# Performance work log

Measured on AMD Instinct MI355X. Metric: run time of the kernel, lower is better.

The kernel has to match this reference:

```python
import jax, jax.numpy as jnp
import numpy as np
from jax import lax

BS, T, D, HID, N = 256, 128, 256, 256, 15


def _gru_layer(x, Wih, Whh, bih, bhh):
    # x: (bs, T, in). PyTorch GRU cell math, gates ordered [r, z, n].
    h0 = jnp.zeros((x.shape[0], Whh.shape[1]), x.dtype)

    def step(h, x_t):
        gi = x_t @ Wih.T + bih
        gh = h @ Whh.T + bhh
        ir, iz, inn = jnp.split(gi, 3, axis=-1)
        hr, hz, hn = jnp.split(gh, 3, axis=-1)
        r = jax.nn.sigmoid(ir + hr)
        z = jax.nn.sigmoid(iz + hz)
        n = jnp.tanh(inn + r * hn)
        h = (1.0 - z) * n + z * h
        return h, h

    _, hs = lax.scan(step, h0, jnp.swapaxes(x, 0, 1))  # (T, bs, H)
    return jnp.swapaxes(hs, 0, 1)


def setup_inputs() -> dict:
    key = jax.random.key(0)
    ks = jax.random.split(key, 14)
    s = 0.08
    inp = {
        'P': jax.random.normal(ks[0], (BS, T, D), jnp.float32),
        'Wih0': jax.random.normal(ks[1], (3 * HID, D), jnp.float32) * s,
        'Whh0': jax.random.normal(ks[2], (3 * HID, HID), jnp.float32) * s,
        'bih0': jax.random.normal(ks[3], (3 * HID,), jnp.float32) * s,
        'bhh0': jax.random.normal(ks[4], (3 * HID,), jnp.float32) * s,
        'Wih1': jax.random.normal(ks[5], (3 * HID, HID), jnp.float32) * s,
        'Whh1': jax.random.normal(ks[6], (3 * HID, HID), jnp.float32) * s,
        'bih1': jax.random.normal(ks[7], (3 * HID,), jnp.float32) * s,
        'bhh1': jax.random.normal(ks[8], (3 * HID,), jnp.float32) * s,
        'W': jax.random.normal(ks[9], (D, HID), jnp.float32) * s,
        'Wp1': jax.random.normal(ks[10], (HID, HID), jnp.float32) * s,
        'Wp2': jax.random.normal(ks[11], (1, HID), jnp.float32) * s,
        'Wr1': jax.random.normal(ks[12], (HID, HID), jnp.float32) * s,
        'Wr2': jax.random.normal(ks[13], (D, HID), jnp.float32) * s,
    }
    # Precomputed derangement negatives: cyclic shift by k in [1, bs-1]
    # guarantees neg_idx[t, n, b] != b (matches the original assert).
    rng = np.random.default_rng(0)
    shifts = rng.integers(1, BS, size=(T - 1, N))
    neg_idx = (np.arange(BS)[None, None, :] + shifts[:, :, None]) % BS
    inp['neg_idx'] = jnp.asarray(neg_idx, jnp.int32)  # (T-1, N, bs)
    return inp


def reference(P, Wih0, Whh0, bih0, bhh0, Wih1, Whh1, bih1, bhh1,
              W, Wp1, Wp2, Wr1, Wr2, neg_idx):
    # 2-layer GRU temporal encoder
    H1 = _gru_layer(P, Wih0, Whh0, bih0, bhh0)
    H = _gru_layer(H1, Wih1, Whh1, bih1, bhh1)  # (bs, T, HID)

    # Contrastive loss over timesteps t = 1..T-1 (vectorized)
    WC = jnp.einsum('bth,dh->btd', H[:, :-1], W)   # W(C_t), (bs, T-1, D)
    Pt = P[:, 1:]                                   # positives, (bs, T-1, D)
    sp = jnp.mean(WC * Pt, axis=-1)                 # (bs, T-1)

    Ptt = jnp.swapaxes(Pt, 0, 1)                    # (T-1, bs, D)
    t_ix = jnp.arange(T - 1)[:, None, None]
    Pn = Ptt[t_ix, neg_idx]                         # (T-1, N, bs, D)
    WCt = jnp.swapaxes(WC, 0, 1)                    # (T-1, bs, D)
    sn = jnp.mean(WCt[:, None] * Pn, axis=-1)       # (T-1, N, bs)

    logits = jnp.concatenate([sp.T[:, None], sn], axis=1)  # (T-1, 1+N, bs)
    pos_ce = jax.nn.log_softmax(logits, axis=1)[:, 0]       # (T-1, bs)
    trend_contrastive_loss = jnp.sum(-jnp.mean(pos_ce, axis=1))

    # alpha from last step
    alpha = jnp.mean((H[:, -2:-1] @ W.T) * P[:, -1:], axis=-1)  # (bs, 1)

    # prediction + reconstruction heads (exact GELU, as nn.GELU default)
    y = jax.nn.gelu(H[:, -1] @ Wp1.T, approximate=False) @ Wp2.T          # (bs, 1)
    R = jax.nn.gelu(jnp.einsum('bth,gh->btg', H, Wr1), approximate=False) @ Wr2.T  # (bs, T, D)

    return H, y, R, alpha, trend_contrastive_loss
```

## Files before the change

kernel.cpp:

```cpp
#include <hip/hip_runtime.h>
#include <hip/hip_bf16.h>
#include <cstdint>
#include <cstddef>

#define BSZ  256
#define TDIM 128
#define DDIM 256
#define HIDN 256
#define G3   768

using bf16x8 = __attribute__((ext_vector_type(8))) short;
using f32x4  = __attribute__((ext_vector_type(4))) float;

__device__ __forceinline__ unsigned short f2bf(float f) {
  union { float f; unsigned u; } x; x.f = f;
  unsigned r = x.u + 0x7FFFu + ((x.u >> 16) & 1u);
  return (unsigned short)(r >> 16);
}
__device__ __forceinline__ float sigm(float x) {
  return __builtin_amdgcn_rcpf(1.f + __expf(-x));
}
__device__ __forceinline__ float tanh_f(float x) {
  float e = __expf(2.f * x);
  return 1.f - 2.f * __builtin_amdgcn_rcpf(e + 1.f);
}
__device__ __forceinline__ float gelu_f(float x) {
  return 0.5f * x * (1.f + erff(x * 0.70710678118654752f));
}

__global__ __launch_bounds__(256) void cvt_bf16(const float* __restrict__ src,
                                                unsigned short* __restrict__ dst, int n4) {
  int i = blockIdx.x * 256 + threadIdx.x;
  if (i >= n4) return;
  float4 v = ((const float4*)src)[i];
  ushort4 o;
  o.x = f2bf(v.x); o.y = f2bf(v.y); o.z = f2bf(v.z); o.w = f2bf(v.w);
  ((ushort4*)dst)[i] = o;
}

__global__ __launch_bounds__(256) void wn_pack(const unsigned short* __restrict__ whh,
                                               unsigned short* __restrict__ wnp) {
  const int i = blockIdx.x * 256 + threadIdx.x;
  const int lane = i & 63, t2 = (i >> 6) & 1, w = (i >> 7) & 7, kk = i >> 10;
  const int m16 = lane & 15, quad = lane >> 4;
  *(bf16x8*)&wnp[(size_t)i * 8] =
      *(const bf16x8*)&whh[(size_t)(512 + w * 32 + t2 * 16 + m16) * 256 + kk * 32 + quad * 8];
}

#if defined(__has_builtin)
#if __has_builtin(__builtin_amdgcn_global_load_lds)
#define HAVE_GLL 1
#endif
#endif
#ifndef HAVE_GLL
#define HAVE_GLL 0
#endif

__device__ __forceinline__ void stage16(const unsigned short* gp,
                                        unsigned short* lbase, int lane) {
#if HAVE_GLL
  __builtin_amdgcn_global_load_lds((const __attribute__((address_space(1))) void*)gp,
                                   (__attribute__((address_space(3))) void*)lbase, 16, 0, 0);
#else
  *(bf16x8*)(lbase + lane * 8) = *(const bf16x8*)gp;
#endif
}

__global__ __launch_bounds__(256) void gemm_bf16(
    const unsigned short* __restrict__ A, int lda,
    const unsigned short* __restrict__ B, int ldb,
    const float* __restrict__ bias,
    float* __restrict__ Cf, unsigned short* __restrict__ Cbf,
    int K, int ldc, int do_gelu)
{
  __shared__ unsigned short As[4096], Bs[4096];
  const int tid = threadIdx.x;
  const int w = tid >> 6, lane = tid & 63;
  const int m16 = lane & 15, quad = lane >> 4;
  const int m0 = blockIdx.y * 128, n0 = blockIdx.x * 128;
  const int wm = w >> 1, wn = w & 1;

  const f32x4 z4 = {0.f, 0.f, 0.f, 0.f};
  f32x4 acc[4][4];
#pragma unroll
  for (int i = 0; i < 4; ++i)
#pragma unroll
    for (int j = 0; j < 4; ++j) acc[i][j] = z4;

  const int nk = K >> 5;
  for (int kk = 0; kk < nk; ++kk) {
#pragma unroll
    for (int i = 0; i < 2; ++i) {
      const int r = i * 64 + lane;
      stage16(A + (size_t)(m0 + r) * lda + kk * 32 + w * 8, &As[w * 1024 + i * 512], lane);
      stage16(B + (size_t)(n0 + r) * ldb + kk * 32 + w * 8, &Bs[w * 1024 + i * 512], lane);
    }
    __syncthreads();
    bf16x8 af[4], bfr[4];
#pragma unroll
    for (int i = 0; i < 4; ++i) {
      af[i]  = *(const bf16x8*)&As[quad * 1024 + (wm * 64 + i * 16 + m16) * 8];
      bfr[i] = *(const bf16x8*)&Bs[quad * 1024 + (wn * 64 + i * 16 + m16) * 8];
    }
#pragma unroll
    for (int i = 0; i < 4; ++i)
#pragma unroll
      for (int j = 0; j < 4; ++j)
        acc[i][j] = __builtin_amdgcn_mfma_f32_16x16x32_bf16(af[i], bfr[j], acc[i][j], 0, 0, 0);
    __syncthreads();
  }

#pragma unroll
  for (int i = 0; i < 4; ++i) {
    const int row0 = m0 + wm * 64 + i * 16 + quad * 4;
#pragma unroll
    for (int j = 0; j < 4; ++j) {
      const int col = n0 + wn * 64 + j * 16 + m16;
#pragma unroll
      for (int rg = 0; rg < 4; ++rg) {
        float v = acc[i][j][rg];
        if (bias) v += bias[col];
        if (do_gelu) v = gelu_f(v);
        const size_t off = (size_t)(row0 + rg) * ldc + col;
        if (Cf)  Cf[off] = v;
        if (Cbf) Cbf[off] = f2bf(v);
      }
    }
  }
}

__global__ __launch_bounds__(512, 2) void gru_rec(
    const float* __restrict__ gi,
    const unsigned short* __restrict__ Whh,
    const unsigned short* __restrict__ Wnp,
    const float* __restrict__ bhh,
    float* __restrict__ Hf,
    unsigned short* __restrict__ Hbf)
{
  __shared__ unsigned short hs[2][16 * 256];
  __shared__ unsigned short wn[65536];
  const int tid = threadIdx.x;
  const int w = tid >> 6, lane = tid & 63;
  const int m16 = lane & 15, quad = lane >> 4;
  const int b0 = blockIdx.x * 16;
  const int colw = w * 32;

  for (int i = tid; i < 16 * 256; i += 512) hs[0][i] = 0;

#pragma unroll
  for (int it = 0; it < 16; ++it)
    stage16(Wnp + (size_t)(it * 512 + w * 64 + lane) * 8,
            &wn[(it * 512 + w * 64) * 8], lane);

  bf16x8 wreg[2][2][8];
#pragma unroll
  for (int g = 0; g < 2; ++g)
#pragma unroll
    for (int t2 = 0; t2 < 2; ++t2)
#pragma unroll
      for (int kk = 0; kk < 8; ++kk)
        wreg[g][t2][kk] = *(const bf16x8*)&Whh[(size_t)(g * 256 + colw + t2 * 16 + m16) * 256
                                                + kk * 32 + quad * 8];

  float bb[3][2];
#pragma unroll
  for (int g = 0; g < 3; ++g)
#pragma unroll
    for (int t2 = 0; t2 < 2; ++t2)
      bb[g][t2] = bhh[g * 256 + colw + t2 * 16 + m16];

  const unsigned short* wnT = &wn[(w * 128 + lane) * 8];

  float hreg[2][4] = {};
  const f32x4 z4 = {0.f, 0.f, 0.f, 0.f};
  __syncthreads();

  for (int t = 0; t < TDIM; ++t) {
    const unsigned short* hsr = hs[t & 1];
    unsigned short*       hsw = hs[(t + 1) & 1];

    float giv[3][2][4];
#pragma unroll
    for (int g = 0; g < 3; ++g)
#pragma unroll
      for (int t2 = 0; t2 < 2; ++t2)
#pragma unroll
        for (int rg = 0; rg < 4; ++rg)
          giv[g][t2][rg] = gi[(size_t)((b0 + quad * 4 + rg) * TDIM + t) * G3
                              + g * 256 + colw + t2 * 16 + m16];

    f32x4 acc[3][2];
#pragma unroll
    for (int g = 0; g < 3; ++g) { acc[g][0] = z4; acc[g][1] = z4; }

#pragma unroll
    for (int kk = 0; kk < 8; ++kk) {
      const int c = kk * 4 + quad;
      const bf16x8 a   = *(const bf16x8*)&hsr[m16 * 256 + ((c ^ m16) * 8)];
      const bf16x8 bn0 = *(const bf16x8*)&wnT[kk * 8192];
      const bf16x8 bn1 = *(const bf16x8*)&wnT[kk * 8192 + 512];
      acc[0][0] = __builtin_amdgcn_mfma_f32_16x16x32_bf16(a, wreg[0][0][kk], acc[0][0], 0, 0, 0);
      acc[0][1] = __builtin_amdgcn_mfma_f32_16x16x32_bf16(a, wreg[0][1][kk], acc[0][1], 0, 0, 0);
      acc[1][0] = __builtin_amdgcn_mfma_f32_16x16x32_bf16(a, wreg[1][0][kk], acc[1][0], 0, 0, 0);
      acc[1][1] = __builtin_amdgcn_mfma_f32_16x16x32_bf16(a, wreg[1][1][kk], acc[1][1], 0, 0, 0);
      acc[2][0] = __builtin_amdgcn_mfma_f32_16x16x32_bf16(a, bn0, acc[2][0], 0, 0, 0);
      acc[2][1] = __builtin_amdgcn_mfma_f32_16x16x32_bf16(a, bn1, acc[2][1], 0, 0, 0);
    }

#pragma unroll
    for (int rg = 0; rg < 4; ++rg) {
      float hh[2];
#pragma unroll
      for (int t2 = 0; t2 < 2; ++t2) {
        const float ghr = acc[0][t2][rg] + bb[0][t2];
        const float ghz = acc[1][t2][rg] + bb[1][t2];
        const float ghn = acc[2][t2][rg] + bb[2][t2];
        const float r = sigm(giv[0][t2][rg] + ghr);
        const float z = sigm(giv[1][t2][rg] + ghz);
        const float n = tanh_f(giv[2][t2][rg] + r * ghn);
        float h = hreg[t2][rg];
        h = n + z * (h - n);
        hreg[t2][rg] = h;
        hh[t2] = h;
      }
      const unsigned short hb0 = f2bf(hh[0]);
      const unsigned short hb1 = f2bf(hh[1]);
      const int row = quad * 4 + rg;
      const int col0 = colw + m16, col1 = col0 + 16;
      hsw[row * 256 + (((col0 >> 3) ^ row) * 8) + (col0 & 7)] = hb0;
      hsw[row * 256 + (((col1 >> 3) ^ row) * 8) + (col1 & 7)] = hb1;
      const size_t gidx = (size_t)((b0 + row) * TDIM + t) * HIDN + col0;
      Hbf[gidx]      = hb0;
      Hbf[gidx + 16] = hb1;
      if (Hf) { Hf[gidx] = hh[0]; Hf[gidx + 16] = hh[1]; }
    }
    __syncthreads();
  }
}

__global__ __launch_bounds__(256) void loss_k(
    const float* __restrict__ WC, const float* __restrict__ P,
    const int* __restrict__ neg, float* __restrict__ alpha, float* __restrict__ loss)
{
  const int t = blockIdx.x;
  const int w = threadIdx.x >> 6, lane = threadIdx.x & 63;
  __shared__ float wls[4];
  float lsum = 0.f;
#pragma unroll 1
  for (int bi = 0; bi < 8; ++bi) {
    const int b = blockIdx.y * 32 + w * 8 + bi;
    const float4 wc4 = *(const float4*)&WC[(size_t)(b * TDIM + t) * DDIM + lane * 4];
    float s[16];
    {
      const float4 p4 = *(const float4*)&P[(size_t)(b * TDIM + t + 1) * DDIM + lane * 4];
      s[0] = wc4.x * p4.x + wc4.y * p4.y + wc4.z * p4.z + wc4.w * p4.w;
    }
#pragma unroll
    for (int n = 0; n < 15; ++n) {
      const int rb = neg[(t * 15 + n) * 256 + b];
      const float4 p4 = *(const float4*)&P[(size_t)(rb * TDIM + t + 1) * DDIM + lane * 4];
      s[n + 1] = wc4.x * p4.x + wc4.y * p4.y + wc4.z * p4.z + wc4.w * p4.w;
    }
#pragma unroll
    for (int n = 0; n < 16; ++n) {
      float v = s[n];
#pragma unroll
      for (int off = 32; off > 0; off >>= 1) v += __shfl_xor(v, off);
      s[n] = v * (1.f / 256.f);
    }
    float mx = s[0];
#pragma unroll
    for (int n = 1; n < 16; ++n) mx = fmaxf(mx, s[n]);
    float se = 0.f;
#pragma unroll
    for (int n = 0; n < 16; ++n) se += __expf(s[n] - mx);
    lsum -= (s[0] - mx - __logf(se));
    if (t == TDIM - 2 && lane == 0) alpha[b] = s[0];
  }
  if (lane == 0) wls[w] = lsum;
  __syncthreads();
  if (threadIdx.x == 0)
    atomicAdd(loss, (wls[0] + wls[1] + wls[2] + wls[3]) * (1.f / 256.f));
}

__global__ __launch_bounds__(256) void y_k(const float* __restrict__ Yh,
                                           const float* __restrict__ Wp2,
                                           float* __restrict__ y) {
  const int w = threadIdx.x >> 6, lane = threadIdx.x & 63;
  const int b = blockIdx.x * 4 + w;
  const float4 a = *(const float4*)&Yh[(size_t)b * 256 + lane * 4];
  const float4 q = *(const float4*)&Wp2[lane * 4];
  float s = a.x * q.x + a.y * q.y + a.z * q.z + a.w * q.w;
#pragma unroll
  for (int off = 32; off > 0; off >>= 1) s += __shfl_xor(s, off);
  if (lane == 0) y[b] = s;
}

extern "C" void kernel_launch(void* const* d_in, const int* in_sizes, int n_in,
                              void* d_out, int out_size, void* d_ws, size_t ws_size,
                              hipStream_t stream) {
  (void)in_sizes; (void)n_in; (void)out_size; (void)ws_size;
  const float* P    = (const float*)d_in[0];
  const float* bih0 = (const float*)d_in[3];
  const float* bhh0 = (const float*)d_in[4];
  const float* bih1 = (const float*)d_in[7];
  const float* bhh1 = (const float*)d_in[8];

  char* ws = (char*)d_ws;
  float*          gi   = (float*)(ws + 0);
  unsigned short* Xbf  = (unsigned short*)(ws + 100663296);
  unsigned short* Pbf  = (unsigned short*)(ws + 117440512);
  float*          WC   = (float*)(ws + 134217728);
  unsigned short* wb   = (unsigned short*)(ws + 167772160);
  unsigned short* wih0b = wb;
  unsigned short* whh0b = wb + 196608;
  unsigned short* wih1b = wb + 393216;
  unsigned short* whh1b = wb + 589824;
  unsigned short* wbW   = wb + 786432;
  unsigned short* wp1b  = wb + 851968;
  unsigned short* wr1b  = wb + 917504;
  unsigned short* wr2b  = wb + 983040;
  float*          Yh   = (float*)(ws + 169869312);

  unsigned short* wnp0 = (unsigned short*)WC;
  unsigned short* wnp1 = wnp0 + 65536;

  float* out  = (float*)d_out;
  float* Hout = out;
  float* Yout = out + 8388608;
  float* Rout = out + 8388864;
  float* Aout = out + 16777472;
  float* Lout = out + 16777728;

  cvt_bf16<<<8192, 256, 0, stream>>>(P, Pbf, 2097152);
  cvt_bf16<<<192, 256, 0, stream>>>((const float*)d_in[1], wih0b, 49152);
  cvt_bf16<<<192, 256, 0, stream>>>((const float*)d_in[2], whh0b, 49152);
  cvt_bf16<<<192, 256, 0, stream>>>((const float*)d_in[5], wih1b, 49152);
  cvt_bf16<<<192, 256, 0, stream>>>((const float*)d_in[6], whh1b, 49152);
  cvt_bf16<<<64, 256, 0, stream>>>((const float*)d_in[9],  wbW,  16384);
  cvt_bf16<<<64, 256, 0, stream>>>((const float*)d_in[10], wp1b, 16384);
  cvt_bf16<<<64, 256, 0, stream>>>((const float*)d_in[12], wr1b, 16384);
  cvt_bf16<<<64, 256, 0, stream>>>((const float*)d_in[13], wr2b, 16384);
  wn_pack<<<32, 256, 0, stream>>>(whh0b, wnp0);
  wn_pack<<<32, 256, 0, stream>>>(whh1b, wnp1);

  dim3 thr(256);
  gemm_bf16<<<dim3(6, 256), thr, 0, stream>>>(Pbf, 256, wih0b, 256, bih0, gi, nullptr, 256, 768, 0);
  gru_rec<<<16, 512, 0, stream>>>(gi, whh0b, wnp0, bhh0, nullptr, Xbf);
  gemm_bf16<<<dim3(6, 256), thr, 0, stream>>>(Xbf, 256, wih1b, 256, bih1, gi, nullptr, 256, 768, 0);
  gru_rec<<<16, 512, 0, stream>>>(gi, whh1b, wnp1, bhh1, Hout, Xbf);
  gemm_bf16<<<dim3(2, 256), thr, 0, stream>>>(Xbf, 256, wbW, 256, nullptr, WC, nullptr, 256, 256, 0);
  gemm_bf16<<<dim3(2, 256), thr, 0, stream>>>(Xbf, 256, wr1b, 256, nullptr, nullptr, Pbf, 256, 256, 1);
  gemm_bf16<<<dim3(2, 256), thr, 0, stream>>>(Pbf, 256, wr2b, 256, nullptr, Rout, nullptr, 256, 256, 0);
  gemm_bf16<<<dim3(2, 2), thr, 0, stream>>>(Xbf + 127 * 256, 32768, wp1b, 256, nullptr, Yh, nullptr, 256, 256, 1);
  y_k<<<64, 256, 0, stream>>>(Yh, (const float*)d_in[11], Yout);

  hipMemsetAsync(Lout, 0, 4, stream);
  loss_k<<<dim3(127, 8), thr, 0, stream>>>(WC, P, (const int*)d_in[14], Aout, Lout);
}
```

Before: 902.9 us.

## Keep all recurrent GRU weights in registers and fold biases into input GEMM

The n-gate recurrent weights now live in registers with the r and z weights, replacing the LDS-staged copy and the wn_pack preprocessing kernels. The hidden biases for the r and z gates are added in the input-projection GEMM epilogue, and the MFMA accumulators start from the precomputed gi values. The gi loads for the next step are issued right after the current step's update, before the barrier. This removes LDS weight reads and per-step bias adds from the serial recurrence, but raises per-thread register use, which could cause spills at 512 threads per block.

New measurement: 1.269 ms. +40.5%, slower.

```diff
diff --git a/kernel.cpp b/kernel.cpp
--- a/kernel.cpp
+++ b/kernel.cpp
@@ -38,15 +38,6 @@
   ((ushort4*)dst)[i] = o;
 }
 
-__global__ __launch_bounds__(256) void wn_pack(const unsigned short* __restrict__ whh,
-                                               unsigned short* __restrict__ wnp) {
-  const int i = blockIdx.x * 256 + threadIdx.x;
-  const int lane = i & 63, t2 = (i >> 6) & 1, w = (i >> 7) & 7, kk = i >> 10;
-  const int m16 = lane & 15, quad = lane >> 4;
-  *(bf16x8*)&wnp[(size_t)i * 8] =
-      *(const bf16x8*)&whh[(size_t)(512 + w * 32 + t2 * 16 + m16) * 256 + kk * 32 + quad * 8];
-}
-
 #if defined(__has_builtin)
 #if __has_builtin(__builtin_amdgcn_global_load_lds)
 #define HAVE_GLL 1
@@ -70,6 +61,7 @@
     const unsigned short* __restrict__ A, int lda,
     const unsigned short* __restrict__ B, int ldb,
     const float* __restrict__ bias,
+    const float* __restrict__ bias2, int b2lim,
     float* __restrict__ Cf, unsigned short* __restrict__ Cbf,
     int K, int ldc, int do_gelu)
 {
@@ -120,6 +112,7 @@
       for (int rg = 0; rg < 4; ++rg) {
         float v = acc[i][j][rg];
         if (bias) v += bias[col];
+        if (bias2 && col < b2lim) v += bias2[col];
         if (do_gelu) v = gelu_f(v);
         const size_t off = (size_t)(row0 + rg) * ldc + col;
         if (Cf)  Cf[off] = v;
@@ -132,13 +125,11 @@
 __global__ __launch_bounds__(512, 2) void gru_rec(
     const float* __restrict__ gi,
     const unsigned short* __restrict__ Whh,
-    const unsigned short* __restrict__ Wnp,
     const float* __restrict__ bhh,
     float* __restrict__ Hf,
     unsigned short* __restrict__ Hbf)
 {
   __shared__ unsigned short hs[2][16 * 256];
-  __shared__ unsigned short wn[65536];
   const int tid = threadIdx.x;
   const int w = tid >> 6, lane = tid & 63;
   const int m16 = lane & 15, quad = lane >> 4;
@@ -147,14 +138,9 @@
 
   for (int i = tid; i < 16 * 256; i += 512) hs[0][i] = 0;
 
-#pragma unroll
-  for (int it = 0; it < 16; ++it)
-    stage16(Wnp + (size_t)(it * 512 + w * 64 + lane) * 8,
-            &wn[(it * 512 + w * 64) * 8], lane);
-
-  bf16x8 wreg[2][2][8];
-#pragma unroll
-  for (int g = 0; g < 2; ++g)
+  bf16x8 wreg[3][2][8];
+#pragma unroll
+  for (int g = 0; g < 3; ++g)
 #pragma unroll
     for (int t2 = 0; t2 < 2; ++t2)
 #pragma unroll
@@ -162,49 +148,45 @@
         wreg[g][t2][kk] = *(const bf16x8*)&Whh[(size_t)(g * 256 + colw + t2 * 16 + m16) * 256
                                                 + kk * 32 + quad * 8];
 
-  float bb[3][2];
-#pragma unroll
-  for (int g = 0; g < 3; ++g)
-#pragma unroll
-    for (int t2 = 0; t2 < 2; ++t2)
-      bb[g][t2] = bhh[g * 256 + colw + t2 * 16 + m16];
-
-  const unsigned short* wnT = &wn[(w * 128 + lane) * 8];
-
+  float bbn[2];
+#pragma unroll
+  for (int t2 = 0; t2 < 2; ++t2) bbn[t2] = bhh[512 + colw + t2 * 16 + m16];
+
+  unsigned goff[4];
+#pragma unroll
+  for (int rg = 0; rg < 4; ++rg)
+    goff[rg] = (unsigned)((b0 + quad * 4 + rg) * TDIM) * G3 + colw + m16;
+
+  f32x4 acc[3][2];
+  float givn[2][4];
   float hreg[2][4] = {};
-  const f32x4 z4 = {0.f, 0.f, 0.f, 0.f};
+
+#pragma unroll
+  for (int rg = 0; rg < 4; ++rg)
+#pragma unroll
+    for (int t2 = 0; t2 < 2; ++t2) {
+      acc[0][t2][rg] = gi[goff[rg] + 0 * 256 + t2 * 16];
+      acc[1][t2][rg] = gi[goff[rg] + 1 * 256 + t2 * 16];
+      givn[t2][rg]   = gi[goff[rg] + 2 * 256 + t2 * 16];
+      acc[2][t2][rg] = 0.f;
+    }
+
   __syncthreads();
 
   for (int t = 0; t < TDIM; ++t) {
     const unsigned short* hsr = hs[t & 1];
     unsigned short*       hsw = hs[(t + 1) & 1];
 
-    float giv[3][2][4];
-#pragma unroll
-    for (int g = 0; g < 3; ++g)
-#pragma unroll
-      for (int t2 = 0; t2 < 2; ++t2)
-#pragma unroll
-        for (int rg = 0; rg < 4; ++rg)
-          giv[g][t2][rg] = gi[(size_t)((b0 + quad * 4 + rg) * TDIM + t) * G3
-                              + g * 256 + colw + t2 * 16 + m16];
-
-    f32x4 acc[3][2];
-#pragma unroll
-    for (int g = 0; g < 3; ++g) { acc[g][0] = z4; acc[g][1] = z4; }
-
 #pragma unroll
     for (int kk = 0; kk < 8; ++kk) {
       const int c = kk * 4 + quad;
-      const bf16x8 a   = *(const bf16x8*)&hsr[m16 * 256 + ((c ^ m16) * 8)];
-      const bf16x8 bn0 = *(const bf16x8*)&wnT[kk * 8192];
-      const bf16x8 bn1 = *(const bf16x8*)&wnT[kk * 8192 + 512];
+      const bf16x8 a = *(const bf16x8*)&hsr[m16 * 256 + ((c ^ m16) * 8)];
       acc[0][0] = __builtin_amdgcn_mfma_f32_16x16x32_bf16(a, wreg[0][0][kk], acc[0][0], 0, 0, 0);
       acc[0][1] = __builtin_amdgcn_mfma_f32_16x16x32_bf16(a, wreg[0][1][kk], acc[0][1], 0, 0, 0);
       acc[1][0] = __builtin_amdgcn_mfma_f32_16x16x32_bf16(a, wreg[1][0][kk], acc[1][0], 0, 0, 0);
       acc[1][1] = __builtin_amdgcn_mfma_f32_16x16x32_bf16(a, wreg[1][1][kk], acc[1][1], 0, 0, 0);
-      acc[2][0] = __builtin_amdgcn_mfma_f32_16x16x32_bf16(a, bn0, acc[2][0], 0, 0, 0);
-      acc[2][1] = __builtin_amdgcn_mfma_f32_16x16x32_bf16(a, bn1, acc[2][1], 0, 0, 0);
+      acc[2][0] = __builtin_amdgcn_mfma_f32_16x16x32_bf16(a, wreg[2][0][kk], acc[2][0], 0, 0, 0);
+      acc[2][1] = __builtin_amdgcn_mfma_f32_16x16x32_bf16(a, wreg[2][1][kk], acc[2][1], 0, 0, 0);
     }
 
 #pragma unroll
@@ -212,12 +194,9 @@
       float hh[2];
 #pragma unroll
       for (int t2 = 0; t2 < 2; ++t2) {
-        const float ghr = acc[0][t2][rg] + bb[0][t2];
-        const float ghz = acc[1][t2][rg] + bb[1][t2];
-        const float ghn = acc[2][t2][rg] + bb[2][t2];
-        const float r = sigm(giv[0][t2][rg] + ghr);
-        const float z = sigm(giv[1][t2][rg] + ghz);
-        const float n = tanh_f(giv[2][t2][rg] + r * ghn);
+        const float r = sigm(acc[0][t2][rg]);
+        const float z = sigm(acc[1][t2][rg]);
+        const float n = tanh_f(givn[t2][rg] + r * (acc[2][t2][rg] + bbn[t2]));
         float h = hreg[t2][rg];
         h = n + z * (h - n);
         hreg[t2][rg] = h;
@@ -234,6 +213,21 @@
       Hbf[gidx + 16] = hb1;
       if (Hf) { Hf[gidx] = hh[0]; Hf[gidx + 16] = hh[1]; }
     }
+
+    if (t + 1 < TDIM) {
+#pragma unroll
+      for (int rg = 0; rg < 4; ++rg) goff[rg] += G3;
+    }
+#pragma unroll
+    for (int rg = 0; rg < 4; ++rg)
+#pragma unroll
+      for (int t2 = 0; t2 < 2; ++t2) {
+        acc[0][t2][rg] = gi[goff[rg] + 0 * 256 + t2 * 16];
+        acc[1][t2][rg] = gi[goff[rg] + 1 * 256 + t2 * 16];
+        givn[t2][rg]   = gi[goff[rg] + 2 * 256 + t2 * 16];
+        acc[2][t2][rg] = 0.f;
+      }
+
     __syncthreads();
   }
 }
@@ -322,9 +316,6 @@
   unsigned short* wr2b  = wb + 983040;
   float*          Yh   = (float*)(ws + 169869312);
 
-  unsigned short* wnp0 = (unsigned short*)WC;
-  unsigned short* wnp1 = wnp0 + 65536;
-
   float* out  = (float*)d_out;
   float* Hout = out;
   float* Yout = out + 8388608;
@@ -341,18 +332,16 @@
   cvt_bf16<<<64, 256, 0, stream>>>((const float*)d_in[10], wp1b, 16384);
   cvt_bf16<<<64, 256, 0, stream>>>((const float*)d_in[12], wr1b, 16384);
   cvt_bf16<<<64, 256, 0, stream>>>((const float*)d_in[13], wr2b, 16384);
-  wn_pack<<<32, 256, 0, stream>>>(whh0b, wnp0);
-  wn_pack<<<32, 256, 0, stream>>>(whh1b, wnp1);
 
   dim3 thr(256);
-  gemm_bf16<<<dim3(6, 256), thr, 0, stream>>>(Pbf, 256, wih0b, 256, bih0, gi, nullptr, 256, 768, 0);
-  gru_rec<<<16, 512, 0, stream>>>(gi, whh0b, wnp0, bhh0, nullptr, Xbf);
-  gemm_bf16<<<dim3(6, 256), thr, 0, stream>>>(Xbf, 256, wih1b, 256, bih1, gi, nullptr, 256, 768, 0);
-  gru_rec<<<16, 512, 0, stream>>>(gi, whh1b, wnp1, bhh1, Hout, Xbf);
-  gemm_bf16<<<dim3(2, 256), thr, 0, stream>>>(Xbf, 256, wbW, 256, nullptr, WC, nullptr, 256, 256, 0);
-  gemm_bf16<<<dim3(2, 256), thr, 0, stream>>>(Xbf, 256, wr1b, 256, nullptr, nullptr, Pbf, 256, 256, 1);
-  gemm_bf16<<<dim3(2, 256), thr, 0, stream>>>(Pbf, 256, wr2b, 256, nullptr, Rout, nullptr, 256, 256, 0);
-  gemm_bf16<<<dim3(2, 2), thr, 0, stream>>>(Xbf + 127 * 256, 32768, wp1b, 256, nullptr, Yh, nullptr, 256, 256, 1);
+  gemm_bf16<<<dim3(6, 256), thr, 0, stream>>>(Pbf, 256, wih0b, 256, bih0, bhh0, 512, gi, nullptr, 256, 768, 0);
+  gru_rec<<<16, 512, 0, stream>>>(gi, whh0b, bhh0, nullptr, Xbf);
+  gemm_bf16<<<dim3(6, 256), thr, 0, stream>>>(Xbf, 256, wih1b, 256, bih1, bhh1, 512, gi, nullptr, 256, 768, 0);
+  gru_rec<<<16, 512, 0, stream>>>(gi, whh1b, bhh1, Hout, Xbf);
+  gemm_bf16<<<dim3(2, 256), thr, 0, stream>>>(Xbf, 256, wbW, 256, nullptr, nullptr, 0, WC, nullptr, 256, 256, 0);
+  gemm_bf16<<<dim3(2, 256), thr, 0, stream>>>(Xbf, 256, wr1b, 256, nullptr, nullptr, 0, nullptr, Pbf, 256, 256, 1);
+  gemm_bf16<<<dim3(2, 256), thr, 0, stream>>>(Pbf, 256, wr2b, 256, nullptr, nullptr, 0, Rout, nullptr, 256, 256, 0);
+  gemm_bf16<<<dim3(2, 2), thr, 0, stream>>>(Xbf + 127 * 256, 32768, wp1b, 256, nullptr, nullptr, 0, Yh, nullptr, 256, 256, 1);
   y_k<<<64, 256, 0, stream>>>(Yh, (const float*)d_in[11], Yout);
 
   hipMemsetAsync(Lout, 0, 4, stream);
```
